# Performance work log

Hardware: AMD Instinct MI355X
Metric: run time of the kernel (lower is better)

Reference implementation:

```python
import jax, jax.numpy as jnp
import numpy as np

V, D, N, E, H = 80000, 300, 32, 64, 4
C = D // H          # per-head out channels (concat -> D)
B, T, U, L = 32, 35, 1024, 3
VG = 50000          # last_idx_globals - last_idx_senses
NEG_SLOPE = 0.2


def setup_inputs() -> dict:
    key = jax.random.key(0)
    ks = jax.random.split(key, 16)
    s = 0.02
    inp = {
        'x_indices': jax.random.randint(ks[0], (B, T, N), 0, V),
        'edge_index': jax.random.randint(ks[1], (B, T, 2, E), 0, N),
        'X': jax.random.normal(ks[2], (V, D), jnp.float32) * s,
        'gat_W': jax.random.normal(ks[3], (D, H * C), jnp.float32) * s,
        'att_src': jax.random.normal(ks[4], (H, C), jnp.float32) * s,
        'att_dst': jax.random.normal(ks[5], (H, C), jnp.float32) * s,
        'gat_bias': jnp.zeros((H * C,), jnp.float32),
        'W_ih0': jax.random.normal(ks[6], (4 * U, 2 * D), jnp.float32) * s,
        'W_ih_rest': jax.random.normal(ks[7], (L - 1, 4 * U, U), jnp.float32) * s,
        'W_hh': jax.random.normal(ks[8], (L, 4 * U, U), jnp.float32) * s,
        'b_ih': jnp.zeros((L, 4 * U), jnp.float32),
        'b_hh': jnp.zeros((L, 4 * U), jnp.float32),
        'lin_W': jax.random.normal(ks[9], (VG, U), jnp.float32) * s,
        'lin_b': jnp.zeros((VG,), jnp.float32),
    }
    return inp


def _gat_node0(X, x_indices, edge_index, gat_W, att_src, att_dst, gat_bias):
    # Batched GATConv over G = B*T tiny subgraphs of fixed size N; dense NxN
    # attention per subgraph is used since N=32 (G*H*N*N ~ 4.6M floats).
    b, t, n = x_indices.shape
    G = b * t
    idx = x_indices.reshape(G, n)
    ei = edge_index.reshape(G, 2, -1)
    x = X[idx]                                   # [G,N,D] embedding gather
    h = (x @ gat_W).reshape(G, n, H, C)          # [G,N,H,C]
    a_s = jnp.einsum('gnhc,hc->gnh', h, att_src)
    a_d = jnp.einsum('gnhc,hc->gnh', h, att_dst)
    # e[g,h,i,j] = leaky_relu(a_dst_i + a_src_j)  (messages j -> i)
    e = a_d.transpose(0, 2, 1)[:, :, :, None] + a_s.transpose(0, 2, 1)[:, :, None, :]
    e = jax.nn.leaky_relu(e, NEG_SLOPE)
    src, dst = ei[:, 0], ei[:, 1]
    g_ar = jnp.arange(G)[:, None]
    adj = jnp.zeros((G, n, n), bool).at[g_ar, dst, src].set(True)
    diag = jnp.arange(n)
    adj = adj.at[:, diag, diag].set(True)        # PyG GATConv adds self-loops
    e = jnp.where(adj[:, None, :, :], e, jnp.float32(-1e9))
    alpha = jax.nn.softmax(e, axis=-1)           # softmax over source nodes j
    out = jnp.einsum('ghij,gjhc->gihc', alpha, h)
    node0 = out[:, 0].reshape(G, H * C) + gat_bias  # only node 0 is consumed
    return node0.reshape(b, t, H * C)


def _lstm_layer(xs, Wi, Wh, bi, bh):
    # xs: [T,B,in]; PyTorch gate order i,f,g,o
    bsz, u = xs.shape[1], Wh.shape[1]
    def step(carry, xt):
        hp, cp = carry
        g = xt @ Wi.T + hp @ Wh.T + (bi + bh)
        i_, f_, gg, o_ = jnp.split(g, 4, axis=-1)
        c = jax.nn.sigmoid(f_) * cp + jax.nn.sigmoid(i_) * jnp.tanh(gg)
        hh = jax.nn.sigmoid(o_) * jnp.tanh(c)
        return (hh, c), hh
    init = (jnp.zeros((bsz, u), xs.dtype), jnp.zeros((bsz, u), xs.dtype))
    _, ys = jax.lax.scan(step, init, xs)
    return ys


def reference(x_indices, edge_index, X, gat_W, att_src, att_dst, gat_bias,
              W_ih0, W_ih_rest, W_hh, b_ih, b_hh, lin_W, lin_b):
    b, t, n = x_indices.shape
    node0 = _gat_node0(X, x_indices, edge_index, gat_W, att_src, att_dst, gat_bias)
    curr_emb = X[x_indices[:, :, 0]]                       # [B,T,D]
    sig = jnp.concatenate([curr_emb, node0], axis=-1)      # [B,T,2D]
    seq = sig.transpose(1, 0, 2)                           # [T,B,2D]
    ys = _lstm_layer(seq, W_ih0, W_hh[0], b_ih[0], b_hh[0])
    for l in range(W_ih_rest.shape[0]):
        ys = _lstm_layer(ys, W_ih_rest[l], W_hh[l + 1], b_ih[l + 1], b_hh[l + 1])
    lstm_out = ys.transpose(1, 0, 2).reshape(b * t, -1)    # [B*T,U]
    logits = lstm_out @ lin_W.T + lin_b                    # [B*T,VG]
    return jax.nn.log_softmax(logits, axis=-1)
```

## Files before the change

kernel.cpp:

```cpp
#include <hip/hip_runtime.h>

#define DEV __device__ __forceinline__

typedef __attribute__((ext_vector_type(8))) short short8;
typedef __attribute__((ext_vector_type(4))) float f32x4;
typedef unsigned short u16;

constexpr int kV = 80000, kD = 300, kNN = 32, kEE = 64, kHH = 4, kCC = 75;
constexpr int kB = 32, kT = 35, kU = 1024, kVG = 50000;
constexpr int kG = kB * kT;
constexpr int kM = kG;

constexpr size_t alignup(size_t x) { return (x + 255) & ~size_t(255); }
constexpr size_t OFF_BAR   = 0;
constexpr size_t OFF_WSRC  = 1024;
constexpr size_t OFF_WDST  = alignup(OFF_WSRC + 1200 * 4);
constexpr size_t OFF_BIAS  = alignup(OFF_WDST + 1200 * 4);
constexpr size_t OFF_SIG   = alignup(OFF_BIAS + 3 * 4096 * 4);
constexpr size_t OFF_WX0   = alignup(OFF_SIG + (size_t)35 * 32 * 640 * 2);
constexpr size_t OFF_WX12  = alignup(OFF_WX0 + (size_t)4096 * 640 * 2);
constexpr size_t OFF_GATES = alignup(OFF_WX12 + (size_t)2 * 4096 * 1024 * 2);
constexpr size_t OFF_HIST  = alignup(OFF_GATES + (size_t)1120 * 4096 * 4);
constexpr size_t OFF_PART  = alignup(OFF_HIST + (size_t)3 * 35 * 32 * 1024 * 2);
constexpr size_t OFF_LSE   = alignup(OFF_PART + (size_t)1120 * 784 * 8);
constexpr size_t OFF_LINWB = alignup(OFF_LSE + 1120 * 4);
constexpr size_t kLinWBytes = (size_t)kVG * 1024 * 2;
constexpr size_t kNeedBW   = OFF_LINWB + kLinWBytes;

DEV u16 f2bf(float f) {
  union { float f; unsigned u; } v; v.f = f;
  unsigned r = v.u + 0x7fffu + ((v.u >> 16) & 1u);
  return (u16)(r >> 16);
}
DEV float fexp(float x) { return __builtin_amdgcn_exp2f(x * 1.4426950408889634f); }
DEV float fsigm(float x) {
  float t = __builtin_amdgcn_exp2f(-1.4426950408889634f * x);
  return __builtin_amdgcn_rcpf(1.f + t);
}
DEV float ftanh(float x) {
  float xc = fminf(fmaxf(x, -20.f), 20.f);
  float t = __builtin_amdgcn_exp2f(2.8853900817779268f * xc);
  return (t - 1.f) * __builtin_amdgcn_rcpf(t + 1.f);
}
DEV f32x4 mfma16(short8 a, short8 b, f32x4 c) {
  return __builtin_amdgcn_mfma_f32_16x16x32_bf16(a, b, c, 0, 0, 0);
}
DEV void store_u16_llc(u16* p, u16 v) {
  unsigned vv = v;
  asm volatile("global_store_short %0, %1, off sc0 sc1"
               :: "v"(p), "v"(vv) : "memory");
}
DEV void gll16(const void* g, void* l) {
  __builtin_amdgcn_global_load_lds(
      (const __attribute__((address_space(1))) unsigned int*)g,
      (__attribute__((address_space(3))) unsigned int*)l, 16, 0, 0);
}
DEV short8 ld8bf(const float* p) {
  float4 a = *(const float4*)p;
  float4 b = *(const float4*)(p + 4);
  u16 t[8] = {f2bf(a.x), f2bf(a.y), f2bf(a.z), f2bf(a.w),
              f2bf(b.x), f2bf(b.y), f2bf(b.z), f2bf(b.w)};
  return *(const short8*)t;
}

__global__ void prep_small(const float* __restrict__ gat_W,
                           const float* __restrict__ att_src,
                           const float* __restrict__ att_dst,
                           const float* __restrict__ b_ih,
                           const float* __restrict__ b_hh,
                           float* __restrict__ ws_src, float* __restrict__ ws_dst,
                           float* __restrict__ bias_sum) {
  int total = 1200 + 1200 + 3 * 4096;
  for (int i = blockIdx.x * blockDim.x + threadIdx.x; i < total; i += gridDim.x * blockDim.x) {
    if (i < 1200) {
      int d = i >> 2, h = i & 3;
      float s = 0.f;
      for (int c = 0; c < kCC; ++c) s += gat_W[d * 300 + h * kCC + c] * att_src[h * kCC + c];
      ws_src[i] = s;
    } else if (i < 2400) {
      int j = i - 1200; int d = j >> 2, h = j & 3;
      float s = 0.f;
      for (int c = 0; c < kCC; ++c) s += gat_W[d * 300 + h * kCC + c] * att_dst[h * kCC + c];
      ws_dst[j] = s;
    } else {
      int j = i - 2400;
      bias_sum[j] = b_ih[j] + b_hh[j];
    }
  }
}

__global__ void wx_prep(const float* __restrict__ W_ih0, u16* __restrict__ wx0) {
  const int n0 = 4096 * 640;
  for (int i = blockIdx.x * blockDim.x + threadIdx.x; i < n0; i += gridDim.x * blockDim.x) {
    int row = i / 640, col = i - row * 640;
    float v = (col < 600) ? W_ih0[row * 600 + col] : 0.f;
    wx0[i] = f2bf(v);
  }
}

__global__ void wb_conv(const float* __restrict__ W, u16* __restrict__ Wb) {
  const long n = (long)kVG * 1024;
  long stride = (long)gridDim.x * blockDim.x * 8;
  for (long i = (long)(blockIdx.x * blockDim.x + threadIdx.x) * 8; i < n; i += stride) {
    float4 a = *(const float4*)(W + i);
    float4 b = *(const float4*)(W + i + 4);
    u16 t[8] = {f2bf(a.x), f2bf(a.y), f2bf(a.z), f2bf(a.w),
                f2bf(b.x), f2bf(b.y), f2bf(b.z), f2bf(b.w)};
    *(uint4*)(Wb + i) = *(const uint4*)t;
  }
}

__global__ void __launch_bounds__(256) gat_kernel(
    const int* __restrict__ x_indices, const int* __restrict__ edge_index,
    const float* __restrict__ X, const float* __restrict__ gat_W,
    const float* __restrict__ gat_bias, const float* __restrict__ ws_src,
    const float* __restrict__ ws_dst, u16* __restrict__ sig) {
  __shared__ float xs[32][301];
  __shared__ float a_s[32][4];
  __shared__ float a_d0[4];
  __shared__ float alpha[4][32];
  __shared__ float xw[4][301];
  __shared__ int allowed[32];
  int g = blockIdx.x, tid = threadIdx.x;
  const int* idx = x_indices + g * 32;
  for (int i = tid; i < 32 * 300; i += 256) {
    int j = i / 300, d2 = i - j * 300;
    xs[j][d2] = X[(size_t)idx[j] * 300 + d2];
  }
  if (tid < 32) allowed[tid] = (tid == 0) ? 1 : 0;
  __syncthreads();
  if (tid < 128) {
    int j = tid >> 2, h = tid & 3;
    float s = 0.f;
    for (int d2 = 0; d2 < 300; ++d2) s += xs[j][d2] * ws_src[d2 * 4 + h];
    a_s[j][h] = s;
  } else if (tid < 132) {
    int h = tid - 128; float s = 0.f;
    for (int d2 = 0; d2 < 300; ++d2) s += xs[0][d2] * ws_dst[d2 * 4 + h];
    a_d0[h] = s;
  } else if (tid >= 192) {
    int e = tid - 192;
    int src = edge_index[g * 128 + e];
    int dst = edge_index[g * 128 + 64 + e];
    if (dst == 0) allowed[src] = 1;
  }
  __syncthreads();
  if (tid < 4) {
    int h = tid;
    float ev[32];
// ... 78 lines not shown
    __builtin_amdgcn_s_barrier();
    __builtin_amdgcn_sched_barrier(0);
    short8 bfr[4];
    #pragma unroll
    for (int nt = 0; nt < 4; ++nt)
      bfr[nt] = *(const short8*)&Bs[cur][wn * 64 + nt * 16 + l15][koff];
    #pragma unroll
    for (int mt = 0; mt < 4; ++mt) {
      short8 af = *(const short8*)&As[cur][wm * 64 + mt * 16 + l15][koff];
      #pragma unroll
      for (int nt = 0; nt < 4; ++nt)
        acc[mt][nt] = mfma16(af, bfr[nt], acc[mt][nt]);
    }
    __builtin_amdgcn_sched_barrier(0);
    __builtin_amdgcn_s_barrier();
  }
  #pragma unroll
  for (int mt = 0; mt < 4; ++mt) {
    #pragma unroll
    for (int r = 0; r < 4; ++r) {
      int m = m0 + wm * 64 + mt * 16 + lhi * 4 + r;
      if (m < kM) {
        float* orow = gates + (size_t)m * 4096;
        #pragma unroll
        for (int nt = 0; nt < 4; ++nt) {
          int n = n0 + wn * 64 + nt * 16 + l15;
          orow[(n & 1023) * 4 + (n >> 10)] = acc[mt][nt][r];
        }
      }
    }
  }
}

__global__ void __launch_bounds__(512, 1) lstm_fused012(
    const float* __restrict__ W_hh,
    const float* __restrict__ W_ih_rest,
    const float* __restrict__ gates,
    const float* __restrict__ bias_sum,
    u16* __restrict__ hist0, u16* __restrict__ hist1, u16* __restrict__ hist2,
    unsigned* __restrict__ flags) {
  const int p = blockIdx.x;
  const int u0 = p * 4;
  const int tid = threadIdx.x;
  const int w = tid >> 6, lane = tid & 63, l15 = lane & 15, lhi = lane >> 4;
  const int khalf = w & 1;
  const int job = w >> 1;
  const int kbase = khalf * 512;
  __shared__ float pred0[2][16][33];
  __shared__ float pred1[4][16][33];
  __shared__ float pred2[4][16][33];

  const int grow = (l15 >> 2) * 1024 + u0 + (l15 & 3);
  size_t rowoff = (size_t)grow * 1024 + kbase + lhi * 8;
  const float* m1;
  const float* m2 = W_ih_rest + (size_t)4096 * 1024 + rowoff;
  if (job == 0)      m1 = W_hh + rowoff;
  else if (job == 1) m1 = W_ih_rest + rowoff;
  else if (job == 2) m1 = W_hh + (size_t)4096 * 1024 + rowoff;
  else               m1 = W_hh + (size_t)2 * 4096 * 1024 + rowoff;
  short8 r1[16], r2[16];
  #pragma unroll
  for (int kk = 0; kk < 16; ++kk) r1[kk] = ld8bf(m1 + kk * 32);
  if (job == 2) {
    #pragma unroll
    for (int kk = 0; kk < 16; ++kk) r2[kk] = ld8bf(m2 + kk * 32);
  }

  const int pw_layer = tid >> 7;
  const int pb = (tid & 127) >> 2, pj = tid & 3;
  float bias_r[4] = {0.f, 0.f, 0.f, 0.f};
  if (pw_layer < 3) {
    #pragma unroll
    for (int g = 0; g < 4; ++g)
      bias_r[g] = bias_sum[pw_layer * 4096 + g * 1024 + u0 + pj];
  }
  float c_reg = 0.f;
  const unsigned* f0p = flags + khalf * 128 + lane;
  __syncthreads();

  for (int s = 0; s < 37; ++s) {
    bool active; const u16* hsrc;
    if (job == 0)      { active = (s >= 1 && s < 35);  hsrc = hist0 + (size_t)(s - 1) * 32 * 1024; }
    else if (job == 1) { active = (s >= 1 && s <= 35); hsrc = hist0 + (size_t)(s - 1) * 32 * 1024; }
    else if (job == 2) { active = (s >= 2 && s <= 36); hsrc = hist1 + (size_t)(s - 2) * 32 * 1024; }
    else               { active = (s >= 3 && s <= 36); hsrc = hist2 + (size_t)(s - 3) * 32 * 1024; }
    if (active) {
      unsigned tgt = (unsigned)s;
      while (!__all((int)((__hip_atomic_load(f0p, __ATOMIC_RELAXED,
                                             __HIP_MEMORY_SCOPE_AGENT) >= tgt) &
                          (__hip_atomic_load(f0p + 64, __ATOMIC_RELAXED,
                                             __HIP_MEMORY_SCOPE_AGENT) >= tgt))))
        __builtin_amdgcn_s_sleep(1);
      asm volatile("" ::: "memory");
    }
    f32x4 a0 = {0,0,0,0}, a1 = {0,0,0,0}, a2 = {0,0,0,0}, a3 = {0,0,0,0};
    if (active) {
      const u16* b0p = hsrc + l15 * 1024 + kbase + lhi * 8;
      const u16* b1p = hsrc + (l15 + 16) * 1024 + kbase + lhi * 8;
      if (job == 2) {
        #pragma unroll
        for (int kk = 0; kk < 16; ++kk) {
          short8 b0 = *(const short8*)(b0p + kk * 32);
          short8 b1 = *(const short8*)(b1p + kk * 32);
          a0 = mfma16(r1[kk], b0, a0);
          a1 = mfma16(r1[kk], b1, a1);
          a2 = mfma16(r2[kk], b0, a2);
          a3 = mfma16(r2[kk], b1, a3);
        }
      } else {
        #pragma unroll
        for (int kk = 0; kk < 16; ++kk) {
          short8 b0 = *(const short8*)(b0p + kk * 32);
          short8 b1 = *(const short8*)(b1p + kk * 32);
          a0 = mfma16(r1[kk], b0, a0);
          a1 = mfma16(r1[kk], b1, a1);
        }
      }
    }
    #pragma unroll
    for (int r = 0; r < 4; ++r) {
      int row = lhi * 4 + r;
      if (job == 0) {
        pred0[khalf][row][l15] = a0[r];      pred0[khalf][row][l15 + 16] = a1[r];
      } else if (job == 1) {
        pred1[khalf][row][l15] = a0[r];      pred1[khalf][row][l15 + 16] = a1[r];
      } else if (job == 2) {
        pred1[2 + khalf][row][l15] = a0[r];  pred1[2 + khalf][row][l15 + 16] = a1[r];
        pred2[khalf][row][l15] = a2[r];      pred2[khalf][row][l15 + 16] = a3[r];
      } else {
        pred2[2 + khalf][row][l15] = a0[r];  pred2[2 + khalf][row][l15 + 16] = a1[r];
      }
    }
    __syncthreads();
    bool act = (pw_layer == 0) ? (s < 35)
             : (pw_layer == 1) ? (s >= 1 && s <= 35)
             : (pw_layer == 2) ? (s >= 2 && s <= 36) : false;
    if (act) {
      float pre[4];
      if (pw_layer == 0) {
        #pragma unroll
        for (int g = 0; g < 4; ++g) {
          int row = g * 4 + pj;
          pre[g] = pred0[0][row][pb] + pred0[1][row][pb];
        }
        float4 gx = ((const float4*)gates)[(size_t)(s * 32 + pb) * 1024 + u0 + pj];
        pre[0] += gx.x; pre[1] += gx.y; pre[2] += gx.z; pre[3] += gx.w;
      } else if (pw_layer == 1) {
        #pragma unroll
        for (int g = 0; g < 4; ++g) {
          int row = g * 4 + pj;
          pre[g] = pred1[0][row][pb] + pred1[1][row][pb] +
                   pred1[2][row][pb] + pred1[3][row][pb];
        }
      } else {
        #pragma unroll
        for (int g = 0; g < 4; ++g) {
          int row = g * 4 + pj;
          pre[g] = pred2[0][row][pb] + pred2[1][row][pb] +
                   pred2[2][row][pb] + pred2[3][row][pb];
        }
      }
      float iv = pre[0] + bias_r[0];
      float fv = pre[1] + bias_r[1];
      float gv = pre[2] + bias_r[2];
      float ov = pre[3] + bias_r[3];
      float cc = fsigm(fv) * c_reg + fsigm(iv) * ftanh(gv);
      float hh = fsigm(ov) * ftanh(cc);
      c_reg = cc;
      int t = s - pw_layer;
      u16* dst = (pw_layer == 0) ? hist0 : (pw_layer == 1) ? hist1 : hist2;
      store_u16_llc(dst + ((size_t)(t * 32 + pb) << 10) + u0 + pj, f2bf(hh));
    }
    __syncthreads();
    if (s < 36 && tid == 0)
      __hip_atomic_store(flags + p, (unsigned)(s + 1),
                         __ATOMIC_RELAXED, __HIP_MEMORY_SCOPE_AGENT);
  }
}

DEV void logits_epilogue(f32x4 (&acc)[4][4], int m0, int n0, int wm, int wn,
                         int l15, int lhi, const float* lin_b,
                         float* out, float2* partials, int bn) {
  float bcol[4]; int ncol[4];
  #pragma unroll
  for (int nt = 0; nt < 4; ++nt) {
    int n = n0 + wn * 64 + nt * 16 + l15;
    ncol[nt] = n;
    bcol[nt] = (n < kVG) ? lin_b[n] : -INFINITY;
  }
  #pragma unroll
  for (int mt = 0; mt < 4; ++mt) {
    #pragma unroll
    for (int r = 0; r < 4; ++r) {
      int m = m0 + wm * 64 + mt * 16 + lhi * 4 + r;
      float v0 = acc[mt][0][r] + bcol[0];
      float v1 = acc[mt][1][r] + bcol[1];
      float v2 = acc[mt][2][r] + bcol[2];
      float v3 = acc[mt][3][r] + bcol[3];
      bool mok = (m < kM);
      if (mok) {
        float* orow = out + (size_t)m * kVG;
        if (ncol[0] < kVG) orow[ncol[0]] = v0;
        if (ncol[1] < kVG) orow[ncol[1]] = v1;
        if (ncol[2] < kVG) orow[ncol[2]] = v2;
        if (ncol[3] < kVG) orow[ncol[3]] = v3;
      }
      float mx = fmaxf(fmaxf(v0, v1), fmaxf(v2, v3));
      #pragma unroll
      for (int d2 = 1; d2 < 16; d2 <<= 1) mx = fmaxf(mx, __shfl_xor(mx, d2, 64));
      float sv = 0.f;
      sv += (v0 > -1e30f) ? fexp(v0 - mx) : 0.f;
      sv += (v1 > -1e30f) ? fexp(v1 - mx) : 0.f;
      sv += (v2 > -1e30f) ? fexp(v2 - mx) : 0.f;
      sv += (v3 > -1e30f) ? fexp(v3 - mx) : 0.f;
      #pragma unroll
      for (int d2 = 1; d2 < 16; d2 <<= 1) sv += __shfl_xor(sv, d2, 64);
      if (mok && l15 == 0)
        partials[(size_t)m * 784 + bn * 2 + wn] = make_float2(mx, sv);
    }
  }
}

__global__ void __launch_bounds__(256, 4) gemm_logits_async(
    const u16* __restrict__ hist2, const u16* __restrict__ linwb,
    const float* __restrict__ lin_b, float* __restrict__ out,
    float2* __restrict__ partials) {
  int nwg = gridDim.x, orig = blockIdx.x;
  int q = nwg >> 3, r = nwg & 7, xcd = orig & 7, off = orig >> 3;
  int bid = (xcd < r ? xcd * (q + 1) : r * (q + 1) + (xcd - r) * q) + off;
  int bm = bid % 9, bn = bid / 9;
  int m0 = bm * 128, n0 = bn * 128;
  int tid = threadIdx.x, w = tid >> 6, lane = tid & 63, l15 = lane & 15, lhi = lane >> 4;
  int wm = w & 1, wn = w >> 1;
  __shared__ u16 As[2][128][32];
  __shared__ u16 Bs[2][128][32];
  int cl = ((lane & 3) ^ ((lane >> 3) & 3)) * 8;
  int am0 = m0 + w * 32 + (lane >> 2);
  int am1 = am0 + 16;
  int mm0 = (am0 < kM) ? am0 : 0, mm1 = (am1 < kM) ? am1 : 0;
  const u16* arow0 = hist2 + (((size_t)((mm0 % 35) * 32 + mm0 / 35)) << 10) + cl;
  const u16* arow1 = hist2 + (((size_t)((mm1 % 35) * 32 + mm1 / 35)) << 10) + cl;
  int nr0 = n0 + w * 32 + (lane >> 2);
  int nn0 = (nr0 < kVG) ? nr0 : 0, nn1 = (nr0 + 16 < kVG) ? nr0 + 16 : 0;
  const u16* brow0 = linwb + ((size_t)nn0 << 10) + cl;
  const u16* brow1 = linwb + ((size_t)nn1 << 10) + cl;
  const int koff = (lhi ^ ((l15 >> 1) & 3)) * 8;

  f32x4 acc[4][4];
  #pragma unroll
  for (int i = 0; i < 4; ++i)
    #pragma unroll
    for (int j = 0; j < 4; ++j) { f32x4 z = {0.f, 0.f, 0.f, 0.f}; acc[i][j] = z; }

  auto ISSUE = [&](int k0, int buf) {
    gll16(arow0 + k0, &As[buf][w * 32][0]);
    gll16(arow1 + k0, &As[buf][w * 32 + 16][0]);
    gll16(brow0 + k0, &Bs[buf][w * 32][0]);
    gll16(brow1 + k0, &Bs[buf][w * 32 + 16][0]);
  };
  ISSUE(0, 0);
  for (int kt = 0; kt < 32; ++kt) {
    int cur = kt & 1;
    if (kt < 31) {
      ISSUE((kt + 1) * 32, cur ^ 1);
      asm volatile("s_waitcnt vmcnt(4)" ::: "memory");
    } else {
      asm volatile("s_waitcnt vmcnt(0)" ::: "memory");
    }
    __builtin_amdgcn_s_barrier();
    __builtin_amdgcn_sched_barrier(0);
    short8 bfr[4];
    #pragma unroll
    for (int nt = 0; nt < 4; ++nt)
      bfr[nt] = *(const short8*)&Bs[cur][wn * 64 + nt * 16 + l15][koff];
    #pragma unroll
    for (int mt = 0; mt < 4; ++mt) {
      short8 af = *(const short8*)&As[cur][wm * 64 + mt * 16 + l15][koff];
      #pragma unroll
      for (int nt = 0; nt < 4; ++nt)
        acc[mt][nt] = mfma16(af, bfr[nt], acc[mt][nt]);
    }
    __builtin_amdgcn_sched_barrier(0);
    __builtin_amdgcn_s_barrier();
  }
  logits_epilogue(acc, m0, n0, wm, wn, l15, lhi, lin_b, out, partials, bn);
}

__global__ void __launch_bounds__(256, 1) gemm_logits_fb(
    const u16* __restrict__ hist2, const float* __restrict__ lin_W,
    const float* __restrict__ lin_b, float* __restrict__ out,
    float2* __restrict__ partials) {
  int nwg = gridDim.x, orig = blockIdx.x;
  int q = nwg >> 3, r = nwg & 7, xcd = orig & 7, off = orig >> 3;
  int bid = (xcd < r ? xcd * (q + 1) : r * (q + 1) + (xcd - r) * q) + off;
  int bm = bid % 9, bn = bid / 9;
  int m0 = bm * 128, n0 = bn * 128;
  int tid = threadIdx.x, w = tid >> 6, lane = tid & 63, l15 = lane & 15, lhi = lane >> 4;
  int wm = w & 1, wn = w >> 1;
  __shared__ u16 As[128][40];
  __shared__ u16 Bs[128][40];
  f32x4 acc[4][4];
  #pragma unroll
  for (int i = 0; i < 4; ++i)
    #pragma unroll
    for (int j = 0; j < 4; ++j) { f32x4 z = {0.f, 0.f, 0.f, 0.f}; acc[i][j] = z; }
  for (int kt = 0; kt < 32; ++kt) {
    int k0 = kt * 32;
    #pragma unroll
    for (int q2 = 0; q2 < 2; ++q2) {
      int c = tid * 2 + q2; int row = c >> 2; int ch = c & 3;
      int m = m0 + row;
      uint4 av{0u, 0u, 0u, 0u};
      if (m < kM) {
        int b = m / 35; int t = m - b * 35;
        av = *(const uint4*)(hist2 + ((size_t)(t * 32 + b) << 10) + k0 + ch * 8);
      }
      *(uint4*)&As[row][ch * 8] = av;
      int n = n0 + row;
      uint4 bv{0u, 0u, 0u, 0u};
      if (n < kVG) {
        const float* src = lin_W + (size_t)n * 1024 + k0 + ch * 8;
        float4 f0 = *(const float4*)(src);
        float4 f1 = *(const float4*)(src + 4);
        bv.x = (unsigned)f2bf(f0.x) | ((unsigned)f2bf(f0.y) << 16);
        bv.y = (unsigned)f2bf(f0.z) | ((unsigned)f2bf(f0.w) << 16);
        bv.z = (unsigned)f2bf(f1.x) | ((unsigned)f2bf(f1.y) << 16);
        bv.w = (unsigned)f2bf(f1.z) | ((unsigned)f2bf(f1.w) << 16);
      }
      *(uint4*)&Bs[row][ch * 8] = bv;
    }
    __syncthreads();
    short8 bfr[4];
    #pragma unroll
    for (int nt = 0; nt < 4; ++nt)
      bfr[nt] = *(const short8*)&Bs[wn * 64 + nt * 16 + l15][lhi * 8];
    #pragma unroll
    for (int mt = 0; mt < 4; ++mt) {
      short8 af = *(const short8*)&As[wm * 64 + mt * 16 + l15][lhi * 8];
      #pragma unroll
      for (int nt = 0; nt < 4; ++nt)
        acc[mt][nt] = mfma16(af, bfr[nt], acc[mt][nt]);
    }
    __syncthreads();
  }
  logits_epilogue(acc, m0, n0, wm, wn, l15, lhi, lin_b, out, partials, bn);
}

__global__ void reduce_rows(const float2* __restrict__ partials, float* __restrict__ lse) {
  int m = blockIdx.x, tid = threadIdx.x;
  float mx = -INFINITY, s = 0.f;
  for (int j = tid; j < 782; j += 256) {
    float2 p = partials[(size_t)m * 784 + j];
    if (p.x > mx) { s = s * fexp(mx - p.x) + p.y; mx = p.x; }
    else          { s += p.y * fexp(p.x - mx); }
  }
  for (int d = 1; d < 64; d <<= 1) {
    float omx = __shfl_xor(mx, d, 64);
    float os  = __shfl_xor(s, d, 64);
    if (omx > mx) { s = s * fexp(mx - omx) + os; mx = omx; }
    else          { s += os * fexp(omx - mx); }
  }
  __shared__ float smx[4], ssum[4];
  int w = tid >> 6;
  if ((tid & 63) == 0) { smx[w] = mx; ssum[w] = s; }
  __syncthreads();
  if (tid == 0) {
    for (int i = 1; i < 4; ++i) {
      float omx = smx[i], os = ssum[i];
      if (omx > mx) { s = s * fexp(mx - omx) + os; mx = omx; }
      else          { s += os * fexp(omx - mx); }
    }
    lse[m] = mx + logf(s);
  }
}

__global__ void sub_lse(float* __restrict__ out, const float* __restrict__ lse) {
  const int total4 = 14000000;
  for (int i = blockIdx.x * blockDim.x + threadIdx.x; i < total4; i += gridDim.x * blockDim.x) {
// ... 11 lines not shown
  const int*   x_indices  = (const int*)d_in[0];
  const int*   edge_index = (const int*)d_in[1];
  const float* X          = (const float*)d_in[2];
  const float* gat_W      = (const float*)d_in[3];
  const float* att_src    = (const float*)d_in[4];
  const float* att_dst    = (const float*)d_in[5];
  const float* gat_bias   = (const float*)d_in[6];
  const float* W_ih0      = (const float*)d_in[7];
  const float* W_ih_rest  = (const float*)d_in[8];
  const float* W_hh       = (const float*)d_in[9];
  const float* b_ih       = (const float*)d_in[10];
  const float* b_hh       = (const float*)d_in[11];
  const float* lin_W      = (const float*)d_in[12];
  const float* lin_b      = (const float*)d_in[13];
  float* out = (float*)d_out;
  char* ws = (char*)d_ws;

  unsigned* flags    = (unsigned*)(ws + OFF_BAR);
  float*    ws_src   = (float*)(ws + OFF_WSRC);
  float*    ws_dst   = (float*)(ws + OFF_WDST);
  float*    bias_sum = (float*)(ws + OFF_BIAS);
  u16*      sig      = (u16*)(ws + OFF_SIG);
  u16*      wx0      = (u16*)(ws + OFF_WX0);
  float*    gates    = (float*)(ws + OFF_GATES);
  u16*      hist     = (u16*)(ws + OFF_HIST);
  float2*   partials = (float2*)(ws + OFF_PART);
  float*    lse      = (float*)(ws + OFF_LSE);
  u16*      linwb    = (u16*)(ws + OFF_LINWB);
  bool use_bw = (ws_size >= kNeedBW);

  u16* hist0 = hist;
  u16* hist1 = hist + (size_t)35 * 32 * 1024;
  u16* hist2 = hist + (size_t)2 * 35 * 32 * 1024;

  hipMemsetAsync(ws + OFF_BAR, 0, 1024, stream);
  prep_small<<<64, 256, 0, stream>>>(gat_W, att_src, att_dst, b_ih, b_hh,
                                     ws_src, ws_dst, bias_sum);
  wx_prep<<<512, 256, 0, stream>>>(W_ih0, wx0);
  if (use_bw) wb_conv<<<2048, 256, 0, stream>>>(lin_W, linwb);
  gat_kernel<<<kG, 256, 0, stream>>>(x_indices, edge_index, X, gat_W, gat_bias,
                                     ws_src, ws_dst, sig);
  gemm_ig<<<288, 256, 0, stream>>>(sig, wx0, gates, 640);
  lstm_fused012<<<256, 512, 0, stream>>>(W_hh, W_ih_rest, gates, bias_sum,
                                         hist0, hist1, hist2, flags);
  if (use_bw)
    gemm_logits_async<<<9 * 391, 256, 0, stream>>>(hist2, linwb, lin_b, out, partials);
  else
    gemm_logits_fb<<<9 * 391, 256, 0, stream>>>(hist2, lin_W, lin_b, out, partials);
  reduce_rows<<<kG, 256, 0, stream>>>(partials, lse);
  sub_lse<<<2048, 256, 0, stream>>>(out, lse);
}
```

Before: 889.9 us.

## Decouple LSTM layers into independent per-wave pipelines with per-layer flags

After: 1.378 ms. 1.55x slower.

```diff
diff --git a/kernel.cpp b/kernel.cpp
--- a/kernel.cpp
+++ b/kernel.cpp
@@ -13,7 +13,7 @@
 
 constexpr size_t alignup(size_t x) { return (x + 255) & ~size_t(255); }
 constexpr size_t OFF_BAR   = 0;
-constexpr size_t OFF_WSRC  = 1024;
+constexpr size_t OFF_WSRC  = 4096;
 constexpr size_t OFF_WDST  = alignup(OFF_WSRC + 1200 * 4);
 constexpr size_t OFF_BIAS  = alignup(OFF_WDST + 1200 * 4);
 constexpr size_t OFF_SIG   = alignup(OFF_BIAS + 3 * 4096 * 4);
@@ -61,6 +61,32 @@
   u16 t[8] = {f2bf(a.x), f2bf(a.y), f2bf(a.z), f2bf(a.w),
               f2bf(b.x), f2bf(b.y), f2bf(b.z), f2bf(b.w)};
   return *(const short8*)t;
+}
+DEV void wait256(const unsigned* F, unsigned tgt, int lane) {
+  while (true) {
+    int ok = (__hip_atomic_load(F + lane, __ATOMIC_RELAXED, __HIP_MEMORY_SCOPE_AGENT) >= tgt) &
+             (__hip_atomic_load(F + 64 + lane, __ATOMIC_RELAXED, __HIP_MEMORY_SCOPE_AGENT) >= tgt) &
+             (__hip_atomic_load(F + 128 + lane, __ATOMIC_RELAXED, __HIP_MEMORY_SCOPE_AGENT) >= tgt) &
+             (__hip_atomic_load(F + 192 + lane, __ATOMIC_RELAXED, __HIP_MEMORY_SCOPE_AGENT) >= tgt);
+    if (__all(ok)) break;
+    __builtin_amdgcn_s_sleep(1);
+  }
+  asm volatile("" ::: "memory");
+}
+DEV void wait256x2(const unsigned* A, unsigned ta, const unsigned* B, unsigned tb, int lane) {
+  while (true) {
+    int ok = (__hip_atomic_load(A + lane, __ATOMIC_RELAXED, __HIP_MEMORY_SCOPE_AGENT) >= ta) &
+             (__hip_atomic_load(A + 64 + lane, __ATOMIC_RELAXED, __HIP_MEMORY_SCOPE_AGENT) >= ta) &
+             (__hip_atomic_load(A + 128 + lane, __ATOMIC_RELAXED, __HIP_MEMORY_SCOPE_AGENT) >= ta) &
+             (__hip_atomic_load(A + 192 + lane, __ATOMIC_RELAXED, __HIP_MEMORY_SCOPE_AGENT) >= ta) &
+             (__hip_atomic_load(B + lane, __ATOMIC_RELAXED, __HIP_MEMORY_SCOPE_AGENT) >= tb) &
+             (__hip_atomic_load(B + 64 + lane, __ATOMIC_RELAXED, __HIP_MEMORY_SCOPE_AGENT) >= tb) &
+             (__hip_atomic_load(B + 128 + lane, __ATOMIC_RELAXED, __HIP_MEMORY_SCOPE_AGENT) >= tb) &
+             (__hip_atomic_load(B + 192 + lane, __ATOMIC_RELAXED, __HIP_MEMORY_SCOPE_AGENT) >= tb);
+    if (__all(ok)) break;
+    __builtin_amdgcn_s_sleep(1);
+  }
+  asm volatile("" ::: "memory");
 }
 
 __global__ void prep_small(const float* __restrict__ gat_W,
@@ -259,149 +285,197 @@
   }
 }
 
-__global__ void __launch_bounds__(512, 1) lstm_fused012(
+__global__ void __launch_bounds__(320, 1) lstm_chain(
     const float* __restrict__ W_hh,
     const float* __restrict__ W_ih_rest,
     const float* __restrict__ gates,
     const float* __restrict__ bias_sum,
     u16* __restrict__ hist0, u16* __restrict__ hist1, u16* __restrict__ hist2,
-    unsigned* __restrict__ flags) {
+    unsigned* __restrict__ F0, unsigned* __restrict__ F1,
+    unsigned* __restrict__ F2) {
   const int p = blockIdx.x;
   const int u0 = p * 4;
   const int tid = threadIdx.x;
-  const int w = tid >> 6, lane = tid & 63, l15 = lane & 15, lhi = lane >> 4;
-  const int khalf = w & 1;
-  const int job = w >> 1;
-  const int kbase = khalf * 512;
-  __shared__ float pred0[2][16][33];
-  __shared__ float pred1[4][16][33];
-  __shared__ float pred2[4][16][33];
-
-  const int grow = (l15 >> 2) * 1024 + u0 + (l15 & 3);
-  size_t rowoff = (size_t)grow * 1024 + kbase + lhi * 8;
-  const float* m1;
-  const float* m2 = W_ih_rest + (size_t)4096 * 1024 + rowoff;
-  if (job == 0)      m1 = W_hh + rowoff;
-  else if (job == 1) m1 = W_ih_rest + rowoff;
-  else if (job == 2) m1 = W_hh + (size_t)4096 * 1024 + rowoff;
-  else               m1 = W_hh + (size_t)2 * 4096 * 1024 + rowoff;
-  short8 r1[16], r2[16];
-  #pragma unroll
-  for (int kk = 0; kk < 16; ++kk) r1[kk] = ld8bf(m1 + kk * 32);
-  if (job == 2) {
-    #pragma unroll
-    for (int kk = 0; kk < 16; ++kk) r2[kk] = ld8bf(m2 + kk * 32);
-  }
-
-  const int pw_layer = tid >> 7;
-  const int pb = (tid & 127) >> 2, pj = tid & 3;
-  float bias_r[4] = {0.f, 0.f, 0.f, 0.f};
-  if (pw_layer < 3) {
-    #pragma unroll
-    for (int g = 0; g < 4; ++g)
-      bias_r[g] = bias_sum[pw_layer * 4096 + g * 1024 + u0 + pj];
-  }
-  float c_reg = 0.f;
-  const unsigned* f0p = flags + khalf * 128 + lane;
+  const int w = tid >> 6, lane = tid & 63;
+  const int c16 = lane & 15, u = lane >> 4;
+
+  __shared__ u16 wlds[4][16][1032];
+  __shared__ float pw[5][2][16][17];
+  __shared__ unsigned prog1, prog2;
+
+  if (tid == 0) { prog1 = 0u; prog2 = 0u; }
+  for (int i = tid; i < 4 * 16 * 128; i += 320) {
+    int mat = i >> 11;
+    int rem = i & 2047;
+    int row = rem >> 7;
+    int k8 = (rem & 127) * 8;
+    size_t off = (size_t)((row >> 2) * 1024 + u0 + (row & 3)) * 1024 + k8;
+    const float* src = (mat == 0) ? W_ih_rest + off
+                     : (mat == 1) ? W_hh + (size_t)4096 * 1024 + off
+                     : (mat == 2) ? W_ih_rest + (size_t)4096 * 1024 + off
+                                  : W_hh + (size_t)2 * 4096 * 1024 + off;
+    short8 v = ld8bf(src);
+    *(short8*)&wlds[mat][row][k8] = v;
+  }
   __syncthreads();
 
-  for (int s = 0; s < 37; ++s) {
-    bool active; const u16* hsrc;
-    if (job == 0)      { active = (s >= 1 && s < 35);  hsrc = hist0 + (size_t)(s - 1) * 32 * 1024; }
-    else if (job == 1) { active = (s >= 1 && s <= 35); hsrc = hist0 + (size_t)(s - 1) * 32 * 1024; }
-    else if (job == 2) { active = (s >= 2 && s <= 36); hsrc = hist1 + (size_t)(s - 2) * 32 * 1024; }
-    else               { active = (s >= 3 && s <= 36); hsrc = hist2 + (size_t)(s - 3) * 32 * 1024; }
-    if (active) {
-      unsigned tgt = (unsigned)s;
-      while (!__all((int)((__hip_atomic_load(f0p, __ATOMIC_RELAXED,
-                                             __HIP_MEMORY_SCOPE_AGENT) >= tgt) &
-                          (__hip_atomic_load(f0p + 64, __ATOMIC_RELAXED,
-                                             __HIP_MEMORY_SCOPE_AGENT) >= tgt))))
-        __builtin_amdgcn_s_sleep(1);
-      asm volatile("" ::: "memory");
-    }
-    f32x4 a0 = {0,0,0,0}, a1 = {0,0,0,0}, a2 = {0,0,0,0}, a3 = {0,0,0,0};
-    if (active) {
-      const u16* b0p = hsrc + l15 * 1024 + kbase + lhi * 8;
-      const u16* b1p = hsrc + (l15 + 16) * 1024 + kbase + lhi * 8;
-      if (job == 2) {
+  if (w == 0) {
+    short8 rw[32];
+    size_t grow = (size_t)((c16 >> 2) * 1024 + u0 + (c16 & 3)) * 1024;
+    #pragma unroll
+    for (int kk = 0; kk < 32; ++kk)
+      rw[kk] = ld8bf(W_hh + grow + kk * 32 + u * 8);
+    float bias_r[4];
+    #pragma unroll
+    for (int g = 0; g < 4; ++g) bias_r[g] = bias_sum[g * 1024 + u0 + u];
+    float cr0 = 0.f, cr1 = 0.f;
+    for (int t = 0; t < 35; ++t) {
+      if (t > 0) {
+        wait256(F0, (unsigned)t, lane);
+        const u16* hp = hist0 + (size_t)(t - 1) * 32768;
+        const u16* b0p = hp + c16 * 1024 + u * 8;
+        const u16* b1p = hp + (c16 + 16) * 1024 + u * 8;
+        f32x4 a0 = {0,0,0,0}, a1 = {0,0,0,0};
         #pragma unroll
-        for (int kk = 0; kk < 16; ++kk) {
-          short8 b0 = *(const short8*)(b0p + kk * 32);
-          short8 b1 = *(const short8*)(b1p + kk * 32);
-          a0 = mfma16(r1[kk], b0, a0);
-          a1 = mfma16(r1[kk], b1, a1);
-          a2 = mfma16(r2[kk], b0, a2);
-          a3 = mfma16(r2[kk], b1, a3);
+        for (int kk = 0; kk < 32; ++kk) {
+          a0 = mfma16(rw[kk], *(const short8*)(b0p + kk * 32), a0);
+          a1 = mfma16(rw[kk], *(const short8*)(b1p + kk * 32), a1);
+        }
+        #pragma unroll
+        for (int r = 0; r < 4; ++r) {
+          pw[0][0][u * 4 + r][c16] = a0[r];
+          pw[0][1][u * 4 + r][c16] = a1[r];
         }
       } else {
         #pragma unroll
-        for (int kk = 0; kk < 16; ++kk) {
-          short8 b0 = *(const short8*)(b0p + kk * 32);
-          short8 b1 = *(const short8*)(b1p + kk * 32);
-          a0 = mfma16(r1[kk], b0, a0);
-          a1 = mfma16(r1[kk], b1, a1);
+        for (int r = 0; r < 4; ++r) {
+          pw[0][0][u * 4 + r][c16] = 0.f;
+          pw[0][1][u * 4 + r][c16] = 0.f;
         }
       }
-    }
-    #pragma unroll
-    for (int r = 0; r < 4; ++r) {
-      int row = lhi * 4 + r;
-      if (job == 0) {
-        pred0[khalf][row][l15] = a0[r];      pred0[khalf][row][l15 + 16] = a1[r];
-      } else if (job == 1) {
-        pred1[khalf][row][l15] = a0[r];      pred1[khalf][row][l15 + 16] = a1[r];
-      } else if (job == 2) {
-        pred1[2 + khalf][row][l15] = a0[r];  pred1[2 + khalf][row][l15 + 16] = a1[r];
-        pred2[khalf][row][l15] = a2[r];      pred2[khalf][row][l15 + 16] = a3[r];
+      asm volatile("s_waitcnt lgkmcnt(0)" ::: "memory");
+      __builtin_amdgcn_sched_barrier(0);
+      float4 gx0 = ((const float4*)gates)[(size_t)(t * 32 + c16) * 1024 + u0 + u];
+      float4 gx1 = ((const float4*)gates)[(size_t)(t * 32 + c16 + 16) * 1024 + u0 + u];
+      float p00 = pw[0][0][u][c16]      + gx0.x + bias_r[0];
+      float p01 = pw[0][0][4 + u][c16]  + gx0.y + bias_r[1];
+      float p02 = pw[0][0][8 + u][c16]  + gx0.z + bias_r[2];
+      float p03 = pw[0][0][12 + u][c16] + gx0.w + bias_r[3];
+      float p10 = pw[0][1][u][c16]      + gx1.x + bias_r[0];
+      float p11 = pw[0][1][4 + u][c16]  + gx1.y + bias_r[1];
+      float p12 = pw[0][1][8 + u][c16]  + gx1.z + bias_r[2];
+      float p13 = pw[0][1][12 + u][c16] + gx1.w + bias_r[3];
+      float cc0 = fsigm(p01) * cr0 + fsigm(p00) * ftanh(p02);
+      float hh0 = fsigm(p03) * ftanh(cc0); cr0 = cc0;
+      float cc1 = fsigm(p11) * cr1 + fsigm(p10) * ftanh(p12);
+      float hh1 = fsigm(p13) * ftanh(cc1); cr1 = cc1;
+      store_u16_llc(hist0 + ((size_t)(t * 32 + c16) << 10) + u0 + u, f2bf(hh0));
+      store_u16_llc(hist0 + ((size_t)(t * 32 + c16 + 16) << 10) + u0 + u, f2bf(hh1));
+      asm volatile("s_waitcnt vmcnt(0)" ::: "memory");
+      if (lane == 0)
+        __hip_atomic_store(F0 + p, (unsigned)(t + 1),
+                           __ATOMIC_RELAXED, __HIP_MEMORY_SCOPE_AGENT);
+    }
+  } else if (w <= 2) {
+    const int bb = (w - 1) * 16;
+    float bias_r[4];
+    #pragma unroll
+    for (int g = 0; g < 4; ++g) bias_r[g] = bias_sum[4096 + g * 1024 + u0 + u];
+    float cr = 0.f;
+    for (int t = 0; t < 35; ++t) {
+      if (t > 0) wait256x2(F0, (unsigned)(t + 1), F1, (unsigned)t, lane);
+      else       wait256(F0, 1u, lane);
+      const u16* xp = hist0 + (size_t)t * 32768;
+      const u16* bxp = xp + (bb + c16) * 1024 + u * 8;
+      f32x4 a = {0,0,0,0};
+      #pragma unroll
+      for (int kk = 0; kk < 32; ++kk)
+        a = mfma16(*(const short8*)&wlds[0][c16][kk * 32 + u * 8],
+                   *(const short8*)(bxp + kk * 32), a);
+      if (t > 0) {
+        const u16* hp = hist1 + (size_t)(t - 1) * 32768;
+        const u16* bhp = hp + (bb + c16) * 1024 + u * 8;
+        #pragma unroll
+        for (int kk = 0; kk < 32; ++kk)
+          a = mfma16(*(const short8*)&wlds[1][c16][kk * 32 + u * 8],
+                     *(const short8*)(bhp + kk * 32), a);
+      }
+      #pragma unroll
+      for (int r = 0; r < 4; ++r) pw[w][0][u * 4 + r][c16] = a[r];
+      asm volatile("s_waitcnt lgkmcnt(0)" ::: "memory");
+      __builtin_amdgcn_sched_barrier(0);
+      float q0 = pw[w][0][u][c16]      + bias_r[0];
+      float q1 = pw[w][0][4 + u][c16]  + bias_r[1];
+      float q2 = pw[w][0][8 + u][c16]  + bias_r[2];
+      float q3 = pw[w][0][12 + u][c16] + bias_r[3];
+      float cc = fsigm(q1) * cr + fsigm(q0) * ftanh(q2);
+      float hh = fsigm(q3) * ftanh(cc); cr = cc;
+      store_u16_llc(hist1 + ((size_t)(t * 32 + bb + c16) << 10) + u0 + u, f2bf(hh));
+      asm volatile("s_waitcnt vmcnt(0)" ::: "memory");
+      if (w == 1) {
+        if (lane == 0)
+          __hip_atomic_store(&prog1, (unsigned)(t + 1),
+                             __ATOMIC_RELEASE, __HIP_MEMORY_SCOPE_WORKGROUP);
       } else {
-        pred2[2 + khalf][row][l15] = a0[r];  pred2[2 + khalf][row][l15 + 16] = a1[r];
-      }
-    }
-    __syncthreads();
-    bool act = (pw_layer == 0) ? (s < 35)
-             : (pw_layer == 1) ? (s >= 1 && s <= 35)
-             : (pw_layer == 2) ? (s >= 2 && s <= 36) : false;
-    if (act) {
-      float pre[4];
-      if (pw_layer == 0) {
+        if (lane == 0) {
+          while (__hip_atomic_load(&prog1, __ATOMIC_ACQUIRE,
+                                   __HIP_MEMORY_SCOPE_WORKGROUP) < (unsigned)(t + 1))
+            __builtin_amdgcn_s_sleep(1);
+          __hip_atomic_store(F1 + p, (unsigned)(t + 1),
+                             __ATOMIC_RELAXED, __HIP_MEMORY_SCOPE_AGENT);
+        }
+      }
+    }
+  } else {
+    const int bb = (w - 3) * 16;
+    float bias_r[4];
+    #pragma unroll
+    for (int g = 0; g < 4; ++g) bias_r[g] = bias_sum[8192 + g * 1024 + u0 + u];
+    float cr = 0.f;
+    for (int t = 0; t < 35; ++t) {
+      if (t > 0) wait256x2(F1, (unsigned)(t + 1), F2, (unsigned)t, lane);
+      else       wait256(F1, 1u, lane);
+      const u16* xp = hist1 + (size_t)t * 32768;
+      const u16* bxp = xp + (bb + c16) * 1024 + u * 8;
+      f32x4 a = {0,0,0,0};
+      #pragma unroll
+      for (int kk = 0; kk < 32; ++kk)
+        a = mfma16(*(const short8*)&wlds[2][c16][kk * 32 + u * 8],
+                   *(const short8*)(bxp + kk * 32), a);
+      if (t > 0) {
+        const u16* hp = hist2 + (size_t)(t - 1) * 32768;
+        const u16* bhp = hp + (bb + c16) * 1024 + u * 8;
         #pragma unroll
-        for (int g = 0; g < 4; ++g) {
-          int row = g * 4 + pj;
-          pre[g] = pred0[0][row][pb] + pred0[1][row][pb];
+        for (int kk = 0; kk < 32; ++kk)
+          a = mfma16(*(const short8*)&wlds[3][c16][kk * 32 + u * 8],
+                     *(const short8*)(bhp + kk * 32), a);
+      }
+      #pragma unroll
+      for (int r = 0; r < 4; ++r) pw[w][0][u * 4 + r][c16] = a[r];
+      asm volatile("s_waitcnt lgkmcnt(0)" ::: "memory");
+      __builtin_amdgcn_sched_barrier(0);
+      float q0 = pw[w][0][u][c16]      + bias_r[0];
+      float q1 = pw[w][0][4 + u][c16]  + bias_r[1];
+      float q2 = pw[w][0][8 + u][c16]  + bias_r[2];
+      float q3 = pw[w][0][12 + u][c16] + bias_r[3];
+      float cc = fsigm(q1) * cr + fsigm(q0) * ftanh(q2);
+      float hh = fsigm(q3) * ftanh(cc); cr = cc;
+      store_u16_llc(hist2 + ((size_t)(t * 32 + bb + c16) << 10) + u0 + u, f2bf(hh));
+      asm volatile("s_waitcnt vmcnt(0)" ::: "memory");
+      if (w == 3) {
+        if (lane == 0)
+          __hip_atomic_store(&prog2, (unsigned)(t + 1),
+                             __ATOMIC_RELEASE, __HIP_MEMORY_SCOPE_WORKGROUP);
+      } else {
+        if (lane == 0) {
+          while (__hip_atomic_load(&prog2, __ATOMIC_ACQUIRE,
+                                   __HIP_MEMORY_SCOPE_WORKGROUP) < (unsigned)(t + 1))
+            __builtin_amdgcn_s_sleep(1);
+          __hip_atomic_store(F2 + p, (unsigned)(t + 1),
+                             __ATOMIC_RELAXED, __HIP_MEMORY_SCOPE_AGENT);
         }
-        float4 gx = ((const float4*)gates)[(size_t)(s * 32 + pb) * 1024 + u0 + pj];
-        pre[0] += gx.x; pre[1] += gx.y; pre[2] += gx.z; pre[3] += gx.w;
-      } else if (pw_layer == 1) {
-        #pragma unroll
-        for (int g = 0; g < 4; ++g) {
-          int row = g * 4 + pj;
-          pre[g] = pred1[0][row][pb] + pred1[1][row][pb] +
-                   pred1[2][row][pb] + pred1[3][row][pb];
-        }
-      } else {
-        #pragma unroll
-        for (int g = 0; g < 4; ++g) {
-          int row = g * 4 + pj;
-          pre[g] = pred2[0][row][pb] + pred2[1][row][pb] +
-                   pred2[2][row][pb] + pred2[3][row][pb];
-        }
-      }
-      float iv = pre[0] + bias_r[0];
-      float fv = pre[1] + bias_r[1];
-      float gv = pre[2] + bias_r[2];
-      float ov = pre[3] + bias_r[3];
-      float cc = fsigm(fv) * c_reg + fsigm(iv) * ftanh(gv);
-      float hh = fsigm(ov) * ftanh(cc);
-      c_reg = cc;
-      int t = s - pw_layer;
-      u16* dst = (pw_layer == 0) ? hist0 : (pw_layer == 1) ? hist1 : hist2;
-      store_u16_llc(dst + ((size_t)(t * 32 + pb) << 10) + u0 + pj, f2bf(hh));
-    }
-    __syncthreads();
-    if (s < 36 && tid == 0)
-      __hip_atomic_store(flags + p, (unsigned)(s + 1),
-                         __ATOMIC_RELAXED, __HIP_MEMORY_SCOPE_AGENT);
+      }
+    }
   }
 }
 
@@ -648,8 +722,11 @@
   u16* hist0 = hist;
   u16* hist1 = hist + (size_t)35 * 32 * 1024;
   u16* hist2 = hist + (size_t)2 * 35 * 32 * 1024;
-
-  hipMemsetAsync(ws + OFF_BAR, 0, 1024, stream);
+  unsigned* F0 = flags;
+  unsigned* F1 = flags + 256;
+  unsigned* F2 = flags + 512;
+
+  hipMemsetAsync(ws + OFF_BAR, 0, 4096, stream);
   prep_small<<<64, 256, 0, stream>>>(gat_W, att_src, att_dst, b_ih, b_hh,
                                      ws_src, ws_dst, bias_sum);
   wx_prep<<<512, 256, 0, stream>>>(W_ih0, wx0);
@@ -657,8 +734,8 @@
   gat_kernel<<<kG, 256, 0, stream>>>(x_indices, edge_index, X, gat_W, gat_bias,
                                      ws_src, ws_dst, sig);
   gemm_ig<<<288, 256, 0, stream>>>(sig, wx0, gates, 640);
-  lstm_fused012<<<256, 512, 0, stream>>>(W_hh, W_ih_rest, gates, bias_sum,
-                                         hist0, hist1, hist2, flags);
+  lstm_chain<<<256, 320, 0, stream>>>(W_hh, W_ih_rest, gates, bias_sum,
+                                      hist0, hist1, hist2, F0, F1, F2);
   if (use_bw)
     gemm_logits_async<<<9 * 391, 256, 0, stream>>>(hist2, linwb, lin_b, out, partials);
   else
```

## Widen logits GEMM tile to 256 columns and fuse weight conversion into GAT launch

Applied to the files above, without the earlier changes.

New measurement: 877.8 us. Within noise of the previous version (-1.4%).

```diff
diff --git a/kernel.cpp b/kernel.cpp
--- a/kernel.cpp
+++ b/kernel.cpp
@@ -89,32 +89,32 @@
   }
 }
 
-__global__ void wx_prep(const float* __restrict__ W_ih0, u16* __restrict__ wx0) {
-  const int n0 = 4096 * 640;
-  for (int i = blockIdx.x * blockDim.x + threadIdx.x; i < n0; i += gridDim.x * blockDim.x) {
-    int row = i / 640, col = i - row * 640;
-    float v = (col < 600) ? W_ih0[row * 600 + col] : 0.f;
-    wx0[i] = f2bf(v);
-  }
-}
-
-__global__ void wb_conv(const float* __restrict__ W, u16* __restrict__ Wb) {
-  const long n = (long)kVG * 1024;
-  long stride = (long)gridDim.x * blockDim.x * 8;
-  for (long i = (long)(blockIdx.x * blockDim.x + threadIdx.x) * 8; i < n; i += stride) {
-    float4 a = *(const float4*)(W + i);
-    float4 b = *(const float4*)(W + i + 4);
-    u16 t[8] = {f2bf(a.x), f2bf(a.y), f2bf(a.z), f2bf(a.w),
-                f2bf(b.x), f2bf(b.y), f2bf(b.z), f2bf(b.w)};
-    *(uint4*)(Wb + i) = *(const uint4*)t;
-  }
-}
-
-__global__ void __launch_bounds__(256) gat_kernel(
+__global__ void __launch_bounds__(256) gat_conv(
     const int* __restrict__ x_indices, const int* __restrict__ edge_index,
     const float* __restrict__ X, const float* __restrict__ gat_W,
     const float* __restrict__ gat_bias, const float* __restrict__ ws_src,
-    const float* __restrict__ ws_dst, u16* __restrict__ sig) {
+    const float* __restrict__ ws_dst, u16* __restrict__ sig,
+    const float* __restrict__ lin_W, u16* __restrict__ linwb,
+    const float* __restrict__ W_ih0, u16* __restrict__ wx0) {
+  if (blockIdx.x >= kG) {
+    long cb = blockIdx.x - kG;
+    long tid0 = cb * 256 + threadIdx.x;
+    long stride = 1024L * 256;
+    if (linwb) {
+      long n8 = ((long)kVG * 1024) >> 3;
+      for (long i = tid0; i < n8; i += stride) {
+        long o = i * 8;
+        short8 v = ld8bf(lin_W + o);
+        *(short8*)(linwb + o) = v;
+      }
+    }
+    const long n0w = 4096 * 640;
+    for (long i = tid0; i < n0w; i += stride) {
+      long row = i / 640, col = i - row * 640;
+      wx0[i] = f2bf(col < 600 ? W_ih0[row * 600 + col] : 0.f);
+    }
+    return;
+  }
   __shared__ float xs[32][301];
   __shared__ float a_s[32][4];
   __shared__ float a_d0[4];
@@ -405,50 +405,7 @@
   }
 }
 
-DEV void logits_epilogue(f32x4 (&acc)[4][4], int m0, int n0, int wm, int wn,
-                         int l15, int lhi, const float* lin_b,
-                         float* out, float2* partials, int bn) {
-  float bcol[4]; int ncol[4];
-  #pragma unroll
-  for (int nt = 0; nt < 4; ++nt) {
-    int n = n0 + wn * 64 + nt * 16 + l15;
-    ncol[nt] = n;
-    bcol[nt] = (n < kVG) ? lin_b[n] : -INFINITY;
-  }
-  #pragma unroll
-  for (int mt = 0; mt < 4; ++mt) {
-    #pragma unroll
-    for (int r = 0; r < 4; ++r) {
-      int m = m0 + wm * 64 + mt * 16 + lhi * 4 + r;
-      float v0 = acc[mt][0][r] + bcol[0];
-      float v1 = acc[mt][1][r] + bcol[1];
-      float v2 = acc[mt][2][r] + bcol[2];
-      float v3 = acc[mt][3][r] + bcol[3];
-      bool mok = (m < kM);
-      if (mok) {
-        float* orow = out + (size_t)m * kVG;
-        if (ncol[0] < kVG) orow[ncol[0]] = v0;
-        if (ncol[1] < kVG) orow[ncol[1]] = v1;
-        if (ncol[2] < kVG) orow[ncol[2]] = v2;
-        if (ncol[3] < kVG) orow[ncol[3]] = v3;
-      }
-      float mx = fmaxf(fmaxf(v0, v1), fmaxf(v2, v3));
-      #pragma unroll
-      for (int d2 = 1; d2 < 16; d2 <<= 1) mx = fmaxf(mx, __shfl_xor(mx, d2, 64));
-      float sv = 0.f;
-      sv += (v0 > -1e30f) ? fexp(v0 - mx) : 0.f;
-      sv += (v1 > -1e30f) ? fexp(v1 - mx) : 0.f;
-      sv += (v2 > -1e30f) ? fexp(v2 - mx) : 0.f;
-      sv += (v3 > -1e30f) ? fexp(v3 - mx) : 0.f;
-      #pragma unroll
-      for (int d2 = 1; d2 < 16; d2 <<= 1) sv += __shfl_xor(sv, d2, 64);
-      if (mok && l15 == 0)
-        partials[(size_t)m * 784 + bn * 2 + wn] = make_float2(mx, sv);
-    }
-  }
-}
-
-__global__ void __launch_bounds__(256, 4) gemm_logits_async(
+__global__ void __launch_bounds__(256, 2) gemm_logits_async(
     const u16* __restrict__ hist2, const u16* __restrict__ linwb,
     const float* __restrict__ lin_b, float* __restrict__ out,
     float2* __restrict__ partials) {
@@ -456,61 +413,105 @@
   int q = nwg >> 3, r = nwg & 7, xcd = orig & 7, off = orig >> 3;
   int bid = (xcd < r ? xcd * (q + 1) : r * (q + 1) + (xcd - r) * q) + off;
   int bm = bid % 9, bn = bid / 9;
-  int m0 = bm * 128, n0 = bn * 128;
+  int m0 = bm * 128, n0 = bn * 256;
   int tid = threadIdx.x, w = tid >> 6, lane = tid & 63, l15 = lane & 15, lhi = lane >> 4;
   int wm = w & 1, wn = w >> 1;
   __shared__ u16 As[2][128][32];
-  __shared__ u16 Bs[2][128][32];
+  __shared__ u16 Bs[2][256][32];
   int cl = ((lane & 3) ^ ((lane >> 3) & 3)) * 8;
   int am0 = m0 + w * 32 + (lane >> 2);
   int am1 = am0 + 16;
   int mm0 = (am0 < kM) ? am0 : 0, mm1 = (am1 < kM) ? am1 : 0;
   const u16* arow0 = hist2 + (((size_t)((mm0 % 35) * 32 + mm0 / 35)) << 10) + cl;
   const u16* arow1 = hist2 + (((size_t)((mm1 % 35) * 32 + mm1 / 35)) << 10) + cl;
-  int nr0 = n0 + w * 32 + (lane >> 2);
-  int nn0 = (nr0 < kVG) ? nr0 : 0, nn1 = (nr0 + 16 < kVG) ? nr0 + 16 : 0;
-  const u16* brow0 = linwb + ((size_t)nn0 << 10) + cl;
-  const u16* brow1 = linwb + ((size_t)nn1 << 10) + cl;
+  const u16* browq[4];
+  #pragma unroll
+  for (int q2 = 0; q2 < 4; ++q2) {
+    int nr = n0 + w * 64 + q2 * 16 + (lane >> 2);
+    int nn = (nr < kVG) ? nr : 0;
+    browq[q2] = linwb + ((size_t)nn << 10) + cl;
+  }
   const int koff = (lhi ^ ((l15 >> 1) & 3)) * 8;
 
-  f32x4 acc[4][4];
+  f32x4 acc[4][8];
   #pragma unroll
   for (int i = 0; i < 4; ++i)
     #pragma unroll
-    for (int j = 0; j < 4; ++j) { f32x4 z = {0.f, 0.f, 0.f, 0.f}; acc[i][j] = z; }
+    for (int j = 0; j < 8; ++j) { f32x4 z = {0.f, 0.f, 0.f, 0.f}; acc[i][j] = z; }
 
   auto ISSUE = [&](int k0, int buf) {
     gll16(arow0 + k0, &As[buf][w * 32][0]);
     gll16(arow1 + k0, &As[buf][w * 32 + 16][0]);
-    gll16(brow0 + k0, &Bs[buf][w * 32][0]);
-    gll16(brow1 + k0, &Bs[buf][w * 32 + 16][0]);
+    #pragma unroll
+    for (int q2 = 0; q2 < 4; ++q2)
+      gll16(browq[q2] + k0, &Bs[buf][w * 64 + q2 * 16][0]);
   };
   ISSUE(0, 0);
   for (int kt = 0; kt < 32; ++kt) {
     int cur = kt & 1;
     if (kt < 31) {
       ISSUE((kt + 1) * 32, cur ^ 1);
-      asm volatile("s_waitcnt vmcnt(4)" ::: "memory");
+      asm volatile("s_waitcnt vmcnt(6)" ::: "memory");
     } else {
       asm volatile("s_waitcnt vmcnt(0)" ::: "memory");
     }
     __builtin_amdgcn_s_barrier();
     __builtin_amdgcn_sched_barrier(0);
-    short8 bfr[4];
-    #pragma unroll
-    for (int nt = 0; nt < 4; ++nt)
-      bfr[nt] = *(const short8*)&Bs[cur][wn * 64 + nt * 16 + l15][koff];
+    short8 bfr[8];
+    #pragma unroll
+    for (int nt = 0; nt < 8; ++nt)
+      bfr[nt] = *(const short8*)&Bs[cur][wn * 128 + nt * 16 + l15][koff];
     #pragma unroll
     for (int mt = 0; mt < 4; ++mt) {
       short8 af = *(const short8*)&As[cur][wm * 64 + mt * 16 + l15][koff];
       #pragma unroll
-      for (int nt = 0; nt < 4; ++nt)
+      for (int nt = 0; nt < 8; ++nt)
         acc[mt][nt] = mfma16(af, bfr[nt], acc[mt][nt]);
     }
     __builtin_amdgcn_sched_barrier(0);
     __builtin_amdgcn_s_barrier();
   }
-  logits_epilogue(acc, m0, n0, wm, wn, l15, lhi, lin_b, out, partials, bn);
+  float bcol[8]; int ncol[8];
+  #pragma unroll
+  for (int nt = 0; nt < 8; ++nt) {
+    int n = n0 + wn * 128 + nt * 16 + l15;
+    ncol[nt] = n;
+    bcol[nt] = (n < kVG) ? lin_b[n] : -INFINITY;
+  }
+  #pragma unroll
+  for (int mt = 0; mt < 4; ++mt) {
+    #pragma unroll
+    for (int r = 0; r < 4; ++r) {
+      int m = m0 + wm * 64 + mt * 16 + lhi * 4 + r;
+      bool mok = (m < kM);
+      float v[8];
+      #pragma unroll
+      for (int nt = 0; nt < 8; ++nt) v[nt] = acc[mt][nt][r] + bcol[nt];
+      if (mok) {
+        float* orow = out + (size_t)m * kVG;
+        #pragma unroll
+        for (int nt = 0; nt < 8; ++nt)
+          if (ncol[nt] < kVG) orow[ncol[nt]] = v[nt];
+      }
+      #pragma unroll
+      for (int half = 0; half < 2; ++half) {
+        float v0 = v[half * 4], v1 = v[half * 4 + 1];
+        float v2 = v[half * 4 + 2], v3 = v[half * 4 + 3];
+        float mx = fmaxf(fmaxf(v0, v1), fmaxf(v2, v3));
+        #pragma unroll
+        for (int d2 = 1; d2 < 16; d2 <<= 1) mx = fmaxf(mx, __shfl_xor(mx, d2, 64));
+        float sv = 0.f;
+        sv += (v0 > -1e30f) ? fexp(v0 - mx) : 0.f;
+        sv += (v1 > -1e30f) ? fexp(v1 - mx) : 0.f;
+        sv += (v2 > -1e30f) ? fexp(v2 - mx) : 0.f;
+        sv += (v3 > -1e30f) ? fexp(v3 - mx) : 0.f;
+        #pragma unroll
+        for (int d2 = 1; d2 < 16; d2 <<= 1) sv += __shfl_xor(sv, d2, 64);
+        if (mok && l15 == 0)
+          partials[(size_t)m * 784 + bn * 4 + wn * 2 + half] = make_float2(mx, sv);
+      }
+    }
+  }
 }
 
 __global__ void __launch_bounds__(256, 1) gemm_logits_fb(
@@ -570,7 +571,44 @@
     }
     __syncthreads();
   }
-  logits_epilogue(acc, m0, n0, wm, wn, l15, lhi, lin_b, out, partials, bn);
+  float bcol[4]; int ncol[4];
+  #pragma unroll
+  for (int nt = 0; nt < 4; ++nt) {
+    int n = n0 + wn * 64 + nt * 16 + l15;
+    ncol[nt] = n;
+    bcol[nt] = (n < kVG) ? lin_b[n] : -INFINITY;
+  }
+  #pragma unroll
+  for (int mt = 0; mt < 4; ++mt) {
+    #pragma unroll
+    for (int r = 0; r < 4; ++r) {
+      int m = m0 + wm * 64 + mt * 16 + lhi * 4 + r;
+      float v0 = acc[mt][0][r] + bcol[0];
+      float v1 = acc[mt][1][r] + bcol[1];
+      float v2 = acc[mt][2][r] + bcol[2];
+      float v3 = acc[mt][3][r] + bcol[3];
+      bool mok = (m < kM);
+      if (mok) {
+        float* orow = out + (size_t)m * kVG;
+        if (ncol[0] < kVG) orow[ncol[0]] = v0;
+        if (ncol[1] < kVG) orow[ncol[1]] = v1;
+        if (ncol[2] < kVG) orow[ncol[2]] = v2;
+        if (ncol[3] < kVG) orow[ncol[3]] = v3;
+      }
+      float mx = fmaxf(fmaxf(v0, v1), fmaxf(v2, v3));
+      #pragma unroll
+      for (int d2 = 1; d2 < 16; d2 <<= 1) mx = fmaxf(mx, __shfl_xor(mx, d2, 64));
+      float sv = 0.f;
+      sv += (v0 > -1e30f) ? fexp(v0 - mx) : 0.f;
+      sv += (v1 > -1e30f) ? fexp(v1 - mx) : 0.f;
+      sv += (v2 > -1e30f) ? fexp(v2 - mx) : 0.f;
+      sv += (v3 > -1e30f) ? fexp(v3 - mx) : 0.f;
+      #pragma unroll
+      for (int d2 = 1; d2 < 16; d2 <<= 1) sv += __shfl_xor(sv, d2, 64);
+      if (mok && l15 == 0)
+        partials[(size_t)m * 784 + bn * 2 + wn] = make_float2(mx, sv);
+    }
+  }
 }
 
 __global__ void reduce_rows(const float2* __restrict__ partials, float* __restrict__ lse) {
@@ -652,15 +690,14 @@
   hipMemsetAsync(ws + OFF_BAR, 0, 1024, stream);
   prep_small<<<64, 256, 0, stream>>>(gat_W, att_src, att_dst, b_ih, b_hh,
                                      ws_src, ws_dst, bias_sum);
-  wx_prep<<<512, 256, 0, stream>>>(W_ih0, wx0);
-  if (use_bw) wb_conv<<<2048, 256, 0, stream>>>(lin_W, linwb);
-  gat_kernel<<<kG, 256, 0, stream>>>(x_indices, edge_index, X, gat_W, gat_bias,
-                                     ws_src, ws_dst, sig);
+  gat_conv<<<kG + 1024, 256, 0, stream>>>(
+      x_indices, edge_index, X, gat_W, gat_bias, ws_src, ws_dst, sig,
+      lin_W, use_bw ? linwb : nullptr, W_ih0, wx0);
   gemm_ig<<<288, 256, 0, stream>>>(sig, wx0, gates, 640);
   lstm_fused012<<<256, 512, 0, stream>>>(W_hh, W_ih_rest, gates, bias_sum,
                                          hist0, hist1, hist2, flags);
   if (use_bw)
-    gemm_logits_async<<<9 * 391, 256, 0, stream>>>(hist2, linwb, lin_b, out, partials);
+    gemm_logits_async<<<9 * 196, 256, 0, stream>>>(hist2, linwb, lin_b, out, partials);
   else
     gemm_logits_fb<<<9 * 391, 256, 0, stream>>>(hist2, lin_W, lin_b, out, partials);
   reduce_rows<<<kG, 256, 0, stream>>>(partials, lse);
```
